# Kernel optimization log

Measured on AMD Instinct MI355X. Metric: run time of the kernel, lower is better.

The kernel has to match this reference:

```python
import jax, jax.numpy as jnp
import numpy as np

HEADS = 16
EPS = 1e-5

def _ln(t):
    # LayerNorm over last axis, no affine params
    mu = jnp.mean(t, axis=-1, keepdims=True)
    var = jnp.var(t, axis=-1, keepdims=True)
    return (t - mu) / jnp.sqrt(var + EPS)

def setup_inputs() -> dict:
    key = jax.random.key(0)
    ks = jax.random.split(key, 8)
    b, n, dim, mlp_dim = 4, 2048, 1024, 4096
    s = lambda d: 1.0 / np.sqrt(d)
    return {
        "x": jax.random.normal(ks[0], (b, n, dim), dtype=jnp.float32),
        "Wqkv": jax.random.uniform(ks[1], (dim, 3 * dim), jnp.float32, -s(dim), s(dim)),
        "W1": jax.random.uniform(ks[2], (dim, mlp_dim), jnp.float32, -s(dim), s(dim)),
        "b1": jax.random.uniform(ks[3], (mlp_dim,), jnp.float32, -s(dim), s(dim)),
        "W2": jax.random.uniform(ks[4], (mlp_dim, dim), jnp.float32, -s(mlp_dim), s(mlp_dim)),
        "b2": jax.random.uniform(ks[5], (dim,), jnp.float32, -s(mlp_dim), s(mlp_dim)),
        "Wout": jax.random.uniform(ks[6], (dim, dim), jnp.float32, -s(dim), s(dim)),
        "bout": jax.random.uniform(ks[7], (dim,), jnp.float32, -s(dim), s(dim)),
    }

def reference(x, Wqkv, W1, b1, W2, b2, Wout, bout):
    b, n, dim = x.shape
    h = HEADS
    d = dim // h
    scale = dim ** (-0.5)  # NOTE: module scales by full dim, not head_dim
    qkv = x @ Wqkv  # [b, n, 3*dim]
    qkv = qkv.reshape(b, n, 3, h, d).transpose(2, 0, 3, 1, 4)  # [3, b, h, n, d]
    q, k, v = qkv[0], qkv[1], qkv[2]
    q, k = _ln(q), _ln(k)
    dots = jnp.einsum('bhid,bhjd->bhij', q, k) * scale
    attn = jax.nn.softmax(dots, axis=-1)
    attn_v = jnp.einsum('bhij,bhjd->bhid', attn, v)
    attn_v = attn_v.transpose(0, 2, 1, 3).reshape(b, n, dim)
    attn_out = attn_v @ Wout + bout
    parallel = jax.nn.gelu(x @ W1 + b1, approximate=False) @ W2 + b2
    return _ln(attn_out + parallel)
```

## Files before the change

### kernel.cpp

```cpp
#include <hip/hip_runtime.h>

typedef __attribute__((ext_vector_type(8))) short s16x8;
typedef __attribute__((ext_vector_type(4))) short s16x4;
typedef __attribute__((ext_vector_type(4))) float f32x4;
typedef __attribute__((ext_vector_type(16))) float f32x16;
typedef __attribute__((ext_vector_type(2))) unsigned uint2v;

#define DEVINL __device__ __forceinline__

DEVINL float b2f(short u){ return __uint_as_float(((unsigned)(unsigned short)u) << 16); }
DEVINL short f2bf(float f){
  unsigned u = __float_as_uint(f);
  u += 0x7fffu + ((u >> 16) & 1u);
  return (short)(u >> 16);
}
DEVINL unsigned pkbf(float a, float b){
  return (unsigned)(unsigned short)f2bf(a) | ((unsigned)(unsigned short)f2bf(b) << 16);
}

#if __has_builtin(__builtin_amdgcn_exp2f)
#define EXP2F __builtin_amdgcn_exp2f
#else
#define EXP2F exp2f
#endif

DEVINL f32x4 mfma32(s16x8 a, s16x8 b, f32x4 c){
  return __builtin_amdgcn_mfma_f32_16x16x32_bf16(a, b, c, 0, 0, 0);
}
DEVINL f32x16 mfma3216(s16x8 a, s16x8 b, f32x16 c){
  return __builtin_amdgcn_mfma_f32_32x32x16_bf16(a, b, c, 0, 0, 0);
}

DEVINL uint2v pl32swap(unsigned a, unsigned b){
#if __has_builtin(__builtin_amdgcn_permlane32_swap)
  return __builtin_amdgcn_permlane32_swap(a, b, false, false);
#else
  asm volatile("v_permlane32_swap_b32 %0, %1" : "+v"(a), "+v"(b));
  uint2v r; r[0] = a; r[1] = b; return r;
#endif
}

typedef const unsigned __attribute__((address_space(1)))* gas1;
typedef unsigned __attribute__((address_space(3)))* las3;
DEVINL void gload16(const short* g, short* l){
  __builtin_amdgcn_global_load_lds((gas1)g, (las3)l, 16, 0, 0);
}

#define CFENCE asm volatile("" ::: "memory")
#define PBAR  do{ CFENCE; __builtin_amdgcn_sched_barrier(0); __builtin_amdgcn_s_barrier(); \
                  __builtin_amdgcn_sched_barrier(0); CFENCE; }while(0)
#define VMW4 asm volatile("s_waitcnt vmcnt(4)" ::: "memory")
#define VMW3 asm volatile("s_waitcnt vmcnt(3)" ::: "memory")
#define VMW0 asm volatile("s_waitcnt vmcnt(0)" ::: "memory")

static const int Bc   = 4;
static const int Nc   = 2048;
static const int DIM  = 1024;
static const int Tc   = Bc * Nc;
static const int MLP  = 4096;
static const int D3   = 3072;

static const size_t OFF_XB    = 0;
static const size_t OFF_WQKVT = OFF_XB    + 16777216;
static const size_t OFF_W1T   = OFF_WQKVT + 6291456;
static const size_t OFF_W2T   = OFF_W1T   + 8388608;
static const size_t OFF_WOUTT = OFF_W2T   + 8388608;
static const size_t OFF_QKV   = OFF_WOUTT + 2097152;
static const size_t OFF_QLN   = OFF_QKV   + 50331648;
static const size_t OFF_KLN   = OFF_QLN   + 16777216;
static const size_t OFF_VT    = OFF_KLN   + 16777216;
static const size_t OFF_ATTNV = OFF_VT    + 16777216;
static const size_t OFF_H     = OFF_QKV;
static const size_t OFF_P2    = OFF_KLN;
static const size_t OFF_A2    = OFF_VT;

__global__ __launch_bounds__(256) void conv_x(const float* __restrict__ x, short* __restrict__ xb){
  size_t i = ((size_t)blockIdx.x * 256 + threadIdx.x) * 8;
  f32x4 v0 = *(const f32x4*)(x + i);
  f32x4 v1 = *(const f32x4*)(x + i + 4);
  s16x8 o;
#pragma unroll
  for (int j = 0; j < 4; ++j){ o[j] = f2bf(v0[j]); o[4+j] = f2bf(v1[j]); }
  *(s16x8*)(xb + i) = o;
}

__global__ __launch_bounds__(256) void transpose_conv(const float* __restrict__ W, short* __restrict__ Wt,
                                                      int K, int N){
  __shared__ float tile[32][33];
  int ntx = N >> 5;
  int tx = blockIdx.x % ntx, ty = blockIdx.x / ntx;
  int r = threadIdx.x >> 3, c = (threadIdx.x & 7) * 4;
  f32x4 v = *(const f32x4*)(W + (size_t)(ty*32 + r)*N + tx*32 + c);
  tile[r][c] = v[0]; tile[r][c+1] = v[1]; tile[r][c+2] = v[2]; tile[r][c+3] = v[3];
  __syncthreads();
  s16x4 o;
#pragma unroll
  for (int j = 0; j < 4; ++j) o[j] = f2bf(tile[c+j][r]);
  *(s16x4*)(Wt + (size_t)(tx*32 + r)*K + ty*32 + c) = o;
}

template<int BM, int ACT>
__global__ __launch_bounds__(512, 2) void gemm8p(const short* __restrict__ A, const short* __restrict__ Bt,
                                                 short* __restrict__ C, const float* __restrict__ bias,
                                                 int M, int N, int K){
  constexpr int MREP = BM/32;
  constexpr int ATOT = (BM==256) ? 32768 : 16384;
  __shared__ short lds[ATOT + 32768];
  short* Ab = lds;
  short* Bb = lds + ATOT;

  const int tid = threadIdx.x;
  const int w = tid >> 6, lane = tid & 63;
  const int lr = lane & 15, g = lane >> 4;
  const int wr = w >> 2, wc = w & 3;
  const int NT = K >> 6;

  const int nbn = N >> 8;
  const int cpx = gridDim.x >> 3;
  const int bid = (int)blockIdx.x;
  const int sw = (bid & 7)*cpx + (bid >> 3);
  const int bm = sw / nbn, bn = sw % nbn;

  const int l2 = lane >> 2;
  const int gsw = ((lane & 3) - ((lane >> 3) & 3)) & 3;
  const int cof = gsw * 8;
  const int qsw8 = (((g + (lr >> 1)) & 3)) * 8;

  const size_t arow = (BM==256) ? (size_t)(bm*256 + (w>>2)*128 + (w&3)*16 + l2)
                                : (size_t)(bm*128 + w*16 + l2);
  const short* ap0 = A  + arow*K + cof;
  const short* bp0 = Bt + (size_t)(bn*256 + w*16 + l2)*K + cof;

  auto stA = [&](int T, int kk, int mh){
    if constexpr (BM==256)
      gload16(ap0 + (size_t)mh*64*K + T*64 + kk*32, Ab + (((T&1)*2+kk)*2+mh)*4096 + w*512);
    else
      gload16(ap0 + T*64 + kk*32, Ab + ((T&1)*2+kk)*4096 + w*512);
  };
  auto stB = [&](int T, int kk, int j){
    gload16(bp0 + (size_t)j*128*K + T*64 + kk*32, Bb + ((T&1)*2+kk)*8192 + j*4096 + w*512);
  };
  auto ldA = [&](int buf, int kk, int mh, int mi)->s16x8{
    const int off = (BM==256) ? (((buf*2+kk)*2+mh)*4096) : ((buf*2+kk)*4096);
    return *(const s16x8*)&Ab[off + (wr*64 + mi*16 + lr)*32 + qsw8];
  };
  auto ldB = [&](int buf, int kk, int ni)->s16x8{
    return *(const s16x8*)&Bb[(buf*2+kk)*8192 + (wc*64 + ni*16 + lr)*32 + qsw8];
  };

  f32x4 acc[MREP][4] = {};

#define MMROW(ai, r) \
  acc[r][0]=mfma32(ai,b0,acc[r][0]); acc[r][1]=mfma32(ai,b1,acc[r][1]); \
  acc[r][2]=mfma32(ai,b2,acc[r][2]); acc[r][3]=mfma32(ai,b3,acc[r][3]);

  if constexpr (BM==256){
    stA(0,0,0); stA(0,0,1); stB(0,0,0); stB(0,0,1);
    stA(0,1,0); stA(0,1,1); stB(0,1,0); stB(0,1,1);
    stA(1,0,0); stA(1,0,1); stB(1,0,0); stB(1,0,1);
    VMW4;
  } else {
    stA(0,0,0); stB(0,0,0); stB(0,0,1);
    stA(0,1,0); stB(0,1,0); stB(0,1,1);
    stA(1,0,0); stB(1,0,0); stB(1,0,1);
    VMW3;
  }
  PBAR;

  for (int t = 0; t < NT; ++t){
    const int buf = t & 1;
    const bool s1 = (t+1 < NT), s2 = (t+2 < NT);

    if constexpr (BM==256){
      {
        s16x8 a0=ldA(buf,0,0,0), a1=ldA(buf,0,0,1), a2=ldA(buf,0,0,2), a3=ldA(buf,0,0,3);
        s16x8 b0=ldB(buf,0,0), b1=ldB(buf,0,1), b2=ldB(buf,0,2), b3=ldB(buf,0,3);
        if (s1){ stA(t+1,1,0); stA(t+1,1,1); }
        PBAR;
        __builtin_amdgcn_s_setprio(1);
        MMROW(a0,0) MMROW(a1,1) MMROW(a2,2) MMROW(a3,3)
        __builtin_amdgcn_s_setprio(0);
        PBAR;
      }
      {
        s16x8 a0=ldA(buf,0,1,0), a1=ldA(buf,0,1,1), a2=ldA(buf,0,1,2), a3=ldA(buf,0,1,3);
        s16x8 b0=ldB(buf,0,0), b1=ldB(buf,0,1), b2=ldB(buf,0,2), b3=ldB(buf,0,3);
        if (s1){ stB(t+1,1,0); stB(t+1,1,1); }
        PBAR;
        __builtin_amdgcn_s_setprio(1);
        MMROW(a0,4) MMROW(a1,5) MMROW(a2,6) MMROW(a3,7)
        __builtin_amdgcn_s_setprio(0);
        PBAR;
      }
      {
        s16x8 a0=ldA(buf,1,0,0), a1=ldA(buf,1,0,1), a2=ldA(buf,1,0,2), a3=ldA(buf,1,0,3);
        s16x8 b0=ldB(buf,1,0), b1=ldB(buf,1,1), b2=ldB(buf,1,2), b3=ldB(buf,1,3);
        if (s2){ stA(t+2,0,0); stA(t+2,0,1); }
        PBAR;
        __builtin_amdgcn_s_setprio(1);
        MMROW(a0,0) MMROW(a1,1) MMROW(a2,2) MMROW(a3,3)
        __builtin_amdgcn_s_setprio(0);
        PBAR;
      }
      {
        s16x8 a0=ldA(buf,1,1,0), a1=ldA(buf,1,1,1), a2=ldA(buf,1,1,2), a3=ldA(buf,1,1,3);
        s16x8 b0=ldB(buf,1,0), b1=ldB(buf,1,1), b2=ldB(buf,1,2), b3=ldB(buf,1,3);
        if (s2){ stB(t+2,0,0); stB(t+2,0,1); }
        PBAR;
        __builtin_amdgcn_s_setprio(1);
        MMROW(a0,4) MMROW(a1,5) MMROW(a2,6) MMROW(a3,7)
        __builtin_amdgcn_s_setprio(0);
        if (s2){ VMW4; } else { VMW0; }
        PBAR;
      }
    } else {
      {
        s16x8 a0=ldA(buf,0,0,0), a1=ldA(buf,0,0,1), a2=ldA(buf,0,0,2), a3=ldA(buf,0,0,3);
        s16x8 b0=ldB(buf,0,0), b1=ldB(buf,0,1), b2=ldB(buf,0,2), b3=ldB(buf,0,3);
        if (s1){ stA(t+1,1,0); stB(t+1,1,0); stB(t+1,1,1); }
        PBAR;
        __builtin_amdgcn_s_setprio(1);
        MMROW(a0,0) MMROW(a1,1) MMROW(a2,2) MMROW(a3,3)
        __builtin_amdgcn_s_setprio(0);
        PBAR;
      }
      {
        s16x8 a0=ldA(buf,1,0,0), a1=ldA(buf,1,0,1), a2=ldA(buf,1,0,2), a3=ldA(buf,1,0,3);
        s16x8 b0=ldB(buf,1,0), b1=ldB(buf,1,1), b2=ldB(buf,1,2), b3=ldB(buf,1,3);
        if (s2){ stA(t+2,0,0); stB(t+2,0,0); stB(t+2,0,1); }
        PBAR;
        __builtin_amdgcn_s_setprio(1);
        MMROW(a0,0) MMROW(a1,1) MMROW(a2,2) MMROW(a3,3)
        __builtin_amdgcn_s_setprio(0);
        if (s2){ VMW3; } else { VMW0; }
        PBAR;
      }
    }
  }
#undef MMROW

#pragma unroll
  for (int ni = 0; ni < 4; ++ni){
    const int col = bn*256 + wc*64 + ni*16 + lr;
    const float bv = bias ? bias[col] : 0.f;
#pragma unroll
    for (int a = 0; a < MREP; ++a){
      const int row0 = bm*BM + wr*(BM/2) + a*16 + 4*g;
      f32x4 v = acc[a][ni];
#pragma unroll
      for (int i = 0; i < 4; ++i){
        float val = v[i] + bv;
        if constexpr (ACT) val = 0.5f*val*(1.f + erff(val*0.70710678118f));
        C[(size_t)(row0+i)*N + col] = f2bf(val);
      }
    }
  }
}

__global__ __launch_bounds__(256) void ln_reorg(const short* __restrict__ qkv, short* __restrict__ qln,
                                                short* __restrict__ kln, short* __restrict__ vtb){
  __shared__ short vtile[64*72];
  int bh = blockIdx.x >> 5, tch = blockIdx.x & 31;
  int b = bh >> 4, h = bh & 15;
  int tq = threadIdx.x >> 2, j = threadIdx.x & 3;
  size_t row = (size_t)b*Nc + tch*64 + tq;
  const short* base = qkv + row*D3 + h*64 + j*16;
  size_t orow = ((size_t)bh*Nc + tch*64 + tq)*64 + j*16;

#pragma unroll
  for (int part = 0; part < 2; ++part){
    const short* src = base + part*DIM;
    s16x8 u0 = *(const s16x8*)src;
    s16x8 u1 = *(const s16x8*)(src + 8);
    float f[16]; float s = 0.f, sq = 0.f;
#pragma unroll
    for (int i = 0; i < 8; ++i){ f[i] = b2f(u0[i]); f[8+i] = b2f(u1[i]); }
#pragma unroll
    for (int i = 0; i < 16; ++i){ s += f[i]; sq += f[i]*f[i]; }
    s  += __shfl_xor(s, 1);  s  += __shfl_xor(s, 2);
    sq += __shfl_xor(sq, 1); sq += __shfl_xor(sq, 2);
    float mu = s * (1.f/64.f);
    float var = sq * (1.f/64.f) - mu*mu;
    float inv = rsqrtf(var + 1e-5f) * (part == 0 ? 0.04508422003f : 1.f);
    s16x8 o0, o1;
#pragma unroll
    for (int i = 0; i < 8; ++i){ o0[i] = f2bf((f[i]-mu)*inv); o1[i] = f2bf((f[8+i]-mu)*inv); }
    short* dst = (part == 0 ? qln : kln) + orow;
    *(s16x8*)dst = o0; *(s16x8*)(dst + 8) = o1;
  }

  s16x8 v0 = *(const s16x8*)(base + 2*DIM);
  s16x8 v1 = *(const s16x8*)(base + 2*DIM + 8);
  *(s16x8*)&vtile[tq*72 + j*16]     = v0;
  *(s16x8*)&vtile[tq*72 + j*16 + 8] = v1;
  __syncthreads();
  s16x8 o0, o1;
#pragma unroll
  for (int i = 0; i < 8; ++i){
    o0[i] = vtile[(j*16 + i)*72 + tq];
    o1[i] = vtile[(j*16 + 8 + i)*72 + tq];
  }
  short* vdst = vtb + ((size_t)bh*64 + tq)*Nc + tch*64 + j*16;
  *(s16x8*)vdst = o0; *(s16x8*)(vdst + 8) = o1;
}

__global__ __launch_bounds__(256) void attn_kern(const short* __restrict__ qln, const short* __restrict__ kln,
                                                 const short* __restrict__ vtb, short* __restrict__ attnv){
  __shared__ short Ks[64*72];
  __shared__ short Vs[64*72];
  int bh = blockIdx.x >> 4, qt = blockIdx.x & 15;
  int b = bh >> 4, h = bh & 15;
  int w = threadIdx.x >> 6, lane = threadIdx.x & 63;
  int lq = lane & 31, hi = lane >> 5;
  int qrow = qt*128 + w*32 + lq;

  const short* qp = qln + ((size_t)bh*Nc + qrow)*64 + hi*8;
  s16x8 qf[4];
#pragma unroll
  for (int m = 0; m < 4; ++m) qf[m] = *(const s16x8*)(qp + m*16);

  f32x16 o0 = {0,0,0,0,0,0,0,0,0,0,0,0,0,0,0,0};
  f32x16 o1 = {0,0,0,0,0,0,0,0,0,0,0,0,0,0,0,0};
  float mrun = -INFINITY, l = 0.f;

  int tr = threadIdx.x >> 2, seg = (threadIdx.x & 3) * 16;
  const short* kbase = kln + ((size_t)bh*Nc + tr)*64 + seg;
  const short* vbase = vtb + ((size_t)bh*64 + tr)*Nc + seg;
  short* ksd = &Ks[tr*72 + seg];
  short* vsd = &Vs[tr*72 + seg];

  for (int kt = 0; kt < Nc; kt += 64){
    const short* ksrc = kbase + (size_t)kt*64;
    *(s16x8*)ksd       = *(const s16x8*)ksrc;
    *(s16x8*)(ksd + 8) = *(const s16x8*)(ksrc + 8);
    const short* vsrc = vbase + kt;
    *(s16x8*)vsd       = *(const s16x8*)vsrc;
    *(s16x8*)(vsd + 8) = *(const s16x8*)(vsrc + 8);
    __syncthreads();

#pragma unroll
    for (int kc = 0; kc < 2; ++kc){
      f32x16 st = {0,0,0,0,0,0,0,0,0,0,0,0,0,0,0,0};
#pragma unroll
      for (int m = 0; m < 4; ++m){
        s16x8 kf = *(const s16x8*)&Ks[(kc*32 + lq)*72 + m*16 + hi*8];
        st = mfma3216(kf, qf[m], st);
      }
      float cmax = st[0];
#pragma unroll
      for (int r = 1; r < 16; ++r) cmax = fmaxf(cmax, st[r]);
      cmax = fmaxf(cmax, __shfl_xor(cmax, 32));
      if (__any(cmax > mrun + 8.f)){
        float mnew = fmaxf(mrun, cmax);
        float fr = EXP2F(mrun - mnew);
        l *= fr;
#pragma unroll
        for (int r = 0; r < 16; ++r){ o0[r] *= fr; o1[r] *= fr; }
        mrun = mnew;
      }
      float p[16];
#pragma unroll
      for (int r = 0; r < 16; ++r){ p[r] = EXP2F(st[r] - mrun); l += p[r]; }

#pragma unroll
      for (int kh = 0; kh < 2; ++kh){
        int r0 = kh*8;
        unsigned wa = pkbf(p[r0+0], p[r0+1]);
        unsigned wb = pkbf(p[r0+4], p[r0+5]);
        unsigned wc2 = pkbf(p[r0+2], p[r0+3]);
        unsigned wd = pkbf(p[r0+6], p[r0+7]);
        uint2v s1 = pl32swap(wa, wb);
        uint2v s2 = pl32swap(wc2, wd);
        union { unsigned u[4]; s16x8 v; } pu;
        pu.u[0] = s1[0]; pu.u[1] = s2[0]; pu.u[2] = s1[1]; pu.u[3] = s2[1];
        s16x8 vf0 = *(const s16x8*)&Vs[ lq      *72 + kc*32 + kh*16 + hi*8];
        s16x8 vf1 = *(const s16x8*)&Vs[(32 + lq)*72 + kc*32 + kh*16 + hi*8];
        o0 = mfma3216(vf0, pu.v, o0);
        o1 = mfma3216(vf1, pu.v, o1);
      }
    }
    __syncthreads();
  }

  l += __shfl_xor(l, 32);
  float inv = 1.f / l;
  short* orow = attnv + ((size_t)(b*Nc + qrow))*DIM + h*64;
#pragma unroll
  for (int r = 0; r < 16; r += 2){
    int dv = (r&3) + 8*(r>>2) + 4*hi;
    *(unsigned*)&orow[dv]      = pkbf(o0[r]*inv, o0[r+1]*inv);
    *(unsigned*)&orow[32 + dv] = pkbf(o1[r]*inv, o1[r+1]*inv);
  }
}

__global__ __launch_bounds__(256) void final_ln(const short* __restrict__ a2, const short* __restrict__ p2,
                                                float* __restrict__ out){
  __shared__ float red[16];
  int row = blockIdx.x, tid = threadIdx.x;
  size_t base = (size_t)row*DIM + tid*4;
  s16x4 a = *(const s16x4*)(a2 + base);
  s16x4 p = *(const s16x4*)(p2 + base);
  float v[4]; float s = 0.f, sq = 0.f;
#pragma unroll
  for (int i = 0; i < 4; ++i){ v[i] = b2f(a[i]) + b2f(p[i]); s += v[i]; sq += v[i]*v[i]; }
#pragma unroll
  for (int m = 1; m < 64; m <<= 1){ s += __shfl_xor(s, m); sq += __shfl_xor(sq, m); }
  int wv = tid >> 6;
  if ((tid & 63) == 0){ red[wv] = s; red[8 + wv] = sq; }
  __syncthreads();
  if (tid == 0){
    float S = red[0] + red[1] + red[2] + red[3];
    float Q = red[8] + red[9] + red[10] + red[11];
    float mu = S * (1.f/1024.f);
    float var = Q * (1.f/1024.f) - mu*mu;
    red[12] = mu; red[13] = rsqrtf(var + 1e-5f);
  }
  __syncthreads();
  float mu = red[12], inv = red[13];
#pragma unroll
  for (int i = 0; i < 4; ++i) out[base + i] = (v[i] - mu) * inv;
}

extern "C" void kernel_launch(void* const* d_in, const int* in_sizes, int n_in,
                              void* d_out, int out_size, void* d_ws, size_t ws_size,
                              hipStream_t stream){
  const float* x    = (const float*)d_in[0];
  const float* Wqkv = (const float*)d_in[1];
  const float* W1   = (const float*)d_in[2];
  const float* b1   = (const float*)d_in[3];
  const float* W2   = (const float*)d_in[4];
  const float* b2   = (const float*)d_in[5];
  const float* Wout = (const float*)d_in[6];
  const float* bout = (const float*)d_in[7];
  float* out = (float*)d_out;
  char* ws = (char*)d_ws;

  short* xb    = (short*)(ws + OFF_XB);
  short* wqkvt = (short*)(ws + OFF_WQKVT);
  short* w1t   = (short*)(ws + OFF_W1T);
  short* w2t   = (short*)(ws + OFF_W2T);
  short* woutt = (short*)(ws + OFF_WOUTT);
  short* qkv   = (short*)(ws + OFF_QKV);
  short* qln   = (short*)(ws + OFF_QLN);
  short* kln   = (short*)(ws + OFF_KLN);
  short* vtb   = (short*)(ws + OFF_VT);
  short* attnv = (short*)(ws + OFF_ATTNV);
  short* hbuf  = (short*)(ws + OFF_H);
  short* p2    = (short*)(ws + OFF_P2);
  short* a2    = (short*)(ws + OFF_A2);

  conv_x<<<4096, 256, 0, stream>>>(x, xb);
  transpose_conv<<<(DIM/32)*(D3/32),  256, 0, stream>>>(Wqkv, wqkvt, DIM, D3);
  transpose_conv<<<(DIM/32)*(MLP/32), 256, 0, stream>>>(W1, w1t, DIM, MLP);
  transpose_conv<<<(MLP/32)*(DIM/32), 256, 0, stream>>>(W2, w2t, MLP, DIM);
  transpose_conv<<<(DIM/32)*(DIM/32), 256, 0, stream>>>(Wout, woutt, DIM, DIM);

  gemm8p<128,0><<<(Tc/128)*(D3/256), 512, 0, stream>>>(xb, wqkvt, qkv, nullptr, Tc, D3, DIM);
  ln_reorg<<<64*32, 256, 0, stream>>>(qkv, qln, kln, vtb);
  attn_kern<<<64*16, 256, 0, stream>>>(qln, kln, vtb, attnv);

  gemm8p<256,1><<<(Tc/256)*(MLP/256), 512, 0, stream>>>(xb, w1t, hbuf, b1, Tc, MLP, DIM);
  gemm8p<128,0><<<(Tc/128)*(DIM/256), 512, 0, stream>>>(hbuf, w2t, p2, b2, Tc, DIM, MLP);
  gemm8p<128,0><<<(Tc/128)*(DIM/256), 512, 0, stream>>>(attnv, woutt, a2, bout, Tc, DIM, DIM);

  final_ln<<<Tc, 256, 0, stream>>>(a2, p2, out);
}
```

Before: 441.0 us.

## Prefetch larger K/V tiles into registers in attention and use native bf16 packing

The attention kernel now stages 128-key tiles of K and V instead of 64-key tiles. The next tile is prefetched into registers while the current one is computed, which halves the number of barriers and hides global load latency. Software bf16 rounding is replaced with the hardware v_cvt_pk_bf16_f32 instruction, and the row max uses v_max3_f32. In the GEMM, B fragments are reused across sub-steps instead of being reloaded. In exchange the kernel uses more registers and LDS, which may reduce occupancy.

```diff
diff --git a/kernel.cpp b/kernel.cpp
--- a/kernel.cpp
+++ b/kernel.cpp
@@ -16,6 +16,14 @@
 }
 DEVINL unsigned pkbf(float a, float b){
   return (unsigned)(unsigned short)f2bf(a) | ((unsigned)(unsigned short)f2bf(b) << 16);
+}
+DEVINL unsigned cvtpk(float lo, float hi){
+  unsigned r;
+  asm("v_cvt_pk_bf16_f32 %0, %1, %2" : "=v"(r) : "v"(lo), "v"(hi));
+  return r;
+}
+DEVINL float max3f(float a, float b, float c){
+  float r; asm("v_max3_f32 %0, %1, %2, %3" : "=v"(r) : "v"(a), "v"(b), "v"(c)); return r;
 }
 
 #if __has_builtin(__builtin_amdgcn_exp2f)
@@ -172,9 +180,10 @@
     const bool s1 = (t+1 < NT), s2 = (t+2 < NT);
 
     if constexpr (BM==256){
-      {
-        s16x8 a0=ldA(buf,0,0,0), a1=ldA(buf,0,0,1), a2=ldA(buf,0,0,2), a3=ldA(buf,0,0,3);
-        s16x8 b0=ldB(buf,0,0), b1=ldB(buf,0,1), b2=ldB(buf,0,2), b3=ldB(buf,0,3);
+      s16x8 a0,a1,a2,a3,b0,b1,b2,b3;
+      {
+        a0=ldA(buf,0,0,0); a1=ldA(buf,0,0,1); a2=ldA(buf,0,0,2); a3=ldA(buf,0,0,3);
+        b0=ldB(buf,0,0); b1=ldB(buf,0,1); b2=ldB(buf,0,2); b3=ldB(buf,0,3);
         if (s1){ stA(t+1,1,0); stA(t+1,1,1); }
         PBAR;
         __builtin_amdgcn_s_setprio(1);
@@ -183,8 +192,7 @@
         PBAR;
       }
       {
-        s16x8 a0=ldA(buf,0,1,0), a1=ldA(buf,0,1,1), a2=ldA(buf,0,1,2), a3=ldA(buf,0,1,3);
-        s16x8 b0=ldB(buf,0,0), b1=ldB(buf,0,1), b2=ldB(buf,0,2), b3=ldB(buf,0,3);
+        a0=ldA(buf,0,1,0); a1=ldA(buf,0,1,1); a2=ldA(buf,0,1,2); a3=ldA(buf,0,1,3);
         if (s1){ stB(t+1,1,0); stB(t+1,1,1); }
         PBAR;
         __builtin_amdgcn_s_setprio(1);
@@ -193,8 +201,8 @@
         PBAR;
       }
       {
-        s16x8 a0=ldA(buf,1,0,0), a1=ldA(buf,1,0,1), a2=ldA(buf,1,0,2), a3=ldA(buf,1,0,3);
-        s16x8 b0=ldB(buf,1,0), b1=ldB(buf,1,1), b2=ldB(buf,1,2), b3=ldB(buf,1,3);
+        a0=ldA(buf,1,0,0); a1=ldA(buf,1,0,1); a2=ldA(buf,1,0,2); a3=ldA(buf,1,0,3);
+        b0=ldB(buf,1,0); b1=ldB(buf,1,1); b2=ldB(buf,1,2); b3=ldB(buf,1,3);
         if (s2){ stA(t+2,0,0); stA(t+2,0,1); }
         PBAR;
         __builtin_amdgcn_s_setprio(1);
@@ -203,8 +211,7 @@
         PBAR;
       }
       {
-        s16x8 a0=ldA(buf,1,1,0), a1=ldA(buf,1,1,1), a2=ldA(buf,1,1,2), a3=ldA(buf,1,1,3);
-        s16x8 b0=ldB(buf,1,0), b1=ldB(buf,1,1), b2=ldB(buf,1,2), b3=ldB(buf,1,3);
+        a0=ldA(buf,1,1,0); a1=ldA(buf,1,1,1); a2=ldA(buf,1,1,2); a3=ldA(buf,1,1,3);
         if (s2){ stB(t+2,0,0); stB(t+2,0,1); }
         PBAR;
         __builtin_amdgcn_s_setprio(1);
@@ -306,13 +313,14 @@
 
 __global__ __launch_bounds__(256) void attn_kern(const short* __restrict__ qln, const short* __restrict__ kln,
                                                  const short* __restrict__ vtb, short* __restrict__ attnv){
-  __shared__ short Ks[64*72];
-  __shared__ short Vs[64*72];
-  int bh = blockIdx.x >> 4, qt = blockIdx.x & 15;
-  int b = bh >> 4, h = bh & 15;
-  int w = threadIdx.x >> 6, lane = threadIdx.x & 63;
-  int lq = lane & 31, hi = lane >> 5;
-  int qrow = qt*128 + w*32 + lq;
+  __shared__ short Ks[128*72];
+  __shared__ short Vs[64*136];
+  const int tid = threadIdx.x;
+  const int bh = blockIdx.x >> 4, qt = blockIdx.x & 15;
+  const int b = bh >> 4, h = bh & 15;
+  const int w = tid >> 6, lane = tid & 63;
+  const int lq = lane & 31, hi = lane >> 5;
+  const int qrow = qt*128 + w*32 + lq;
 
   const short* qp = qln + ((size_t)bh*Nc + qrow)*64 + hi*8;
   s16x8 qf[4];
@@ -323,32 +331,51 @@
   f32x16 o1 = {0,0,0,0,0,0,0,0,0,0,0,0,0,0,0,0};
   float mrun = -INFINITY, l = 0.f;
 
-  int tr = threadIdx.x >> 2, seg = (threadIdx.x & 3) * 16;
-  const short* kbase = kln + ((size_t)bh*Nc + tr)*64 + seg;
-  const short* vbase = vtb + ((size_t)bh*64 + tr)*Nc + seg;
-  short* ksd = &Ks[tr*72 + seg];
-  short* vsd = &Vs[tr*72 + seg];
-
-  for (int kt = 0; kt < Nc; kt += 64){
-    const short* ksrc = kbase + (size_t)kt*64;
-    *(s16x8*)ksd       = *(const s16x8*)ksrc;
-    *(s16x8*)(ksd + 8) = *(const s16x8*)(ksrc + 8);
-    const short* vsrc = vbase + kt;
-    *(s16x8*)vsd       = *(const s16x8*)vsrc;
-    *(s16x8*)(vsd + 8) = *(const s16x8*)(vsrc + 8);
+  const short* kb0 = kln + (size_t)bh*Nc*64;
+  const short* vb0 = vtb + (size_t)bh*64*Nc;
+  const int vrow = tid >> 2, vq = tid & 3;
+
+  s16x8 kr[4], vr[4];
+#pragma unroll
+  for (int j = 0; j < 4; ++j){
+    kr[j] = *(const s16x8*)(kb0 + (size_t)(tid + j*256)*8);
+    vr[j] = *(const s16x8*)(vb0 + (size_t)vrow*Nc + (vq + 4*j)*8);
+  }
+
+  for (int kt = 0; kt < 16; ++kt){
+#pragma unroll
+    for (int j = 0; j < 4; ++j){
+      int s = tid + j*256;
+      *(s16x8*)&Ks[(s>>3)*72 + (s&7)*8] = kr[j];
+      *(s16x8*)&Vs[vrow*136 + (vq + 4*j)*8] = vr[j];
+    }
     __syncthreads();
-
-#pragma unroll
-    for (int kc = 0; kc < 2; ++kc){
+    if (kt + 1 < 16){
+      const short* kb = kb0 + (size_t)(kt+1)*128*64;
+      const short* vb = vb0 + (kt+1)*128;
+#pragma unroll
+      for (int j = 0; j < 4; ++j){
+        kr[j] = *(const s16x8*)(kb + (size_t)(tid + j*256)*8);
+        vr[j] = *(const s16x8*)(vb + (size_t)vrow*Nc + (vq + 4*j)*8);
+      }
+    }
+
+#pragma unroll
+    for (int kc = 0; kc < 4; ++kc){
       f32x16 st = {0,0,0,0,0,0,0,0,0,0,0,0,0,0,0,0};
 #pragma unroll
       for (int m = 0; m < 4; ++m){
         s16x8 kf = *(const s16x8*)&Ks[(kc*32 + lq)*72 + m*16 + hi*8];
         st = mfma3216(kf, qf[m], st);
       }
-      float cmax = st[0];
-#pragma unroll
-      for (int r = 1; r < 16; ++r) cmax = fmaxf(cmax, st[r]);
+      float cmax = max3f(st[0], st[1], st[2]);
+      cmax = max3f(cmax, st[3], st[4]);
+      cmax = max3f(cmax, st[5], st[6]);
+      cmax = max3f(cmax, st[7], st[8]);
+      cmax = max3f(cmax, st[9], st[10]);
+      cmax = max3f(cmax, st[11], st[12]);
+      cmax = max3f(cmax, st[13], st[14]);
+      cmax = fmaxf(cmax, st[15]);
       cmax = fmaxf(cmax, __shfl_xor(cmax, 32));
       if (__any(cmax > mrun + 8.f)){
         float mnew = fmaxf(mrun, cmax);
@@ -365,16 +392,16 @@
 #pragma unroll
       for (int kh = 0; kh < 2; ++kh){
         int r0 = kh*8;
-        unsigned wa = pkbf(p[r0+0], p[r0+1]);
-        unsigned wb = pkbf(p[r0+4], p[r0+5]);
-        unsigned wc2 = pkbf(p[r0+2], p[r0+3]);
-        unsigned wd = pkbf(p[r0+6], p[r0+7]);
+        unsigned wa = cvtpk(p[r0+0], p[r0+1]);
+        unsigned wb = cvtpk(p[r0+4], p[r0+5]);
+        unsigned wc2 = cvtpk(p[r0+2], p[r0+3]);
+        unsigned wd = cvtpk(p[r0+6], p[r0+7]);
         uint2v s1 = pl32swap(wa, wb);
         uint2v s2 = pl32swap(wc2, wd);
         union { unsigned u[4]; s16x8 v; } pu;
         pu.u[0] = s1[0]; pu.u[1] = s2[0]; pu.u[2] = s1[1]; pu.u[3] = s2[1];
-        s16x8 vf0 = *(const s16x8*)&Vs[ lq      *72 + kc*32 + kh*16 + hi*8];
-        s16x8 vf1 = *(const s16x8*)&Vs[(32 + lq)*72 + kc*32 + kh*16 + hi*8];
+        s16x8 vf0 = *(const s16x8*)&Vs[ lq      *136 + kc*32 + kh*16 + hi*8];
+        s16x8 vf1 = *(const s16x8*)&Vs[(32 + lq)*136 + kc*32 + kh*16 + hi*8];
         o0 = mfma3216(vf0, pu.v, o0);
         o1 = mfma3216(vf1, pu.v, o1);
       }
@@ -388,8 +415,8 @@
 #pragma unroll
   for (int r = 0; r < 16; r += 2){
     int dv = (r&3) + 8*(r>>2) + 4*hi;
-    *(unsigned*)&orow[dv]      = pkbf(o0[r]*inv, o0[r+1]*inv);
-    *(unsigned*)&orow[32 + dv] = pkbf(o1[r]*inv, o1[r+1]*inv);
+    *(unsigned*)&orow[dv]      = cvtpk(o0[r]*inv, o0[r+1]*inv);
+    *(unsigned*)&orow[32 + dv] = cvtpk(o1[r]*inv, o1[r+1]*inv);
   }
 }
 
```

Result: faster. 419.6 us (-4.9%).
